# Kernel optimization log

Hardware: AMD Instinct MI355X
Metric: run time of the kernel (lower is better)

Reference implementation:

```python
import jax, jax.numpy as jnp
import numpy as np

N = 16000      # points
K = 16         # neighbors per query (fixed-degree CSR)
M = N * K      # attention pairs
C = 384        # embed_dim
H = 6          # num_heads
HD = C // H    # head_dim = 64
L = 25         # quant_grid_length = window/quant = 6.0/0.24
T2 = 2 * L - 1 # rel-pos table length = 49
WIN = 6.0
QUANT = 0.24
SCALE = HD ** -0.5


def setup_inputs() -> dict:
    key = jax.random.key(0)
    ks = jax.random.split(key, 12)
    feats = jax.random.normal(ks[0], (N, C), jnp.float32)
    xyz = jax.random.uniform(ks[1], (N, 3), jnp.float32) * 240.0
    index_0 = jnp.repeat(jnp.arange(N, dtype=jnp.int32), K)            # sorted query ids per pair
    index_0_offsets = jnp.arange(0, M + 1, K, dtype=jnp.int32)         # CSR offsets
    index_1 = jax.random.randint(ks[2], (M,), 0, N, jnp.int32)         # key ids per pair
    sort_idx = jax.random.permutation(ks[3], N).astype(jnp.int32)
    lin = lambda k: jax.random.normal(k, (C, C), jnp.float32) * 0.02
    tab = lambda k: jax.random.normal(k, (T2, 3, H, HD), jnp.float32) * 0.02
    return {
        'feats': feats, 'xyz': xyz,
        'index_0': index_0, 'index_0_offsets': index_0_offsets,
        'index_1': index_1, 'sort_idx': sort_idx,
        'Wq': lin(ks[4]), 'bq': jnp.zeros((C,), jnp.float32),
        'Wk': lin(ks[5]), 'bk': jnp.zeros((C,), jnp.float32),
        'Wv': lin(ks[6]), 'bv': jnp.zeros((C,), jnp.float32),
        'Wp': lin(ks[7]), 'bp': jnp.zeros((C,), jnp.float32),
        'Tq': tab(ks[8]), 'Tk': tab(ks[9]), 'Tv': tab(ks[10]),
    }


def reference(feats, xyz, index_0, index_0_offsets, index_1, sort_idx,
              Wq, bq, Wk, bk, Wv, bv, Wp, bp, Tq, Tk, Tv):
    n = feats.shape[0]
    # QKV projections (key/value default to query feats in the module)
    q = (feats @ Wq.T + bq).reshape(n, H, HD) * SCALE
    k = (feats @ Wk.T + bk).reshape(n, H, HD)
    v = (feats @ Wv.T + bv).reshape(n, H, HD)
    # sort into contiguous-window order
    qs, ks_, vs = q[sort_idx], k[sort_idx], v[sort_idx]
    xyz_s = xyz[sort_idx]
    # quantized in-window coords (shift_win=False -> shift 0)
    xq = jnp.floor(((xyz_s - xyz_s.min(0)) % WIN) / QUANT)             # [N,3], values in [0, L-1]
    i0, i1 = index_0, index_1
    rel_idx = (xq[i0] - xq[i1]).astype(jnp.int32) + (L - 1)            # [M,3] in [0, 2L-2]
    # attention logits: q.k plus contextual relative-position terms
    attn = jnp.einsum('mhd,mhd->mh', qs[i0], ks_[i1])                  # [M,H]
    for t in range(3):
        dq = jnp.einsum('nhd,lhd->nlh', qs, Tq[:, t])                  # [N,T2,H]
        dk = jnp.einsum('nhd,lhd->nlh', ks_, Tk[:, t])
        attn = attn + dq[i0, rel_idx[:, t]] + dk[i1, rel_idx[:, t]]
    # scatter softmax over CSR segments (segments given by index_0)
    amax = jax.ops.segment_max(attn, i0, num_segments=n)
    e = jnp.exp(attn - amax[i0])
    denom = jax.ops.segment_sum(e, i0, num_segments=n)
    a = e / denom[i0]                                                  # [M,H]
    # weighted value aggregation
    x = jax.ops.segment_sum(a[:, :, None] * vs[i1], i0, num_segments=n)  # [N,H,HD]
    # relative-position value contribution, factored through table bins
    for t in range(3):
        seg2 = i0 * T2 + rel_idx[:, t]
        w = jax.ops.segment_sum(a, seg2, num_segments=n * T2).reshape(n, T2, H)
        x = x + jnp.einsum('nlh,lhd->nhd', w, Tv[:, t])
    # unsort back to input order and project
    out = jnp.zeros_like(x).at[sort_idx].set(x).reshape(n, C)
    return out @ Wp.T + bp
```

## Files before the change

### kernel.cpp

```cpp
#include <hip/hip_runtime.h>
#include <hip/hip_bf16.h>
#include <cstdint>
#include <cstddef>

#define NPTS 16000
#define KNB  16
#define CDIM 384
#define NH   6
#define HDIM 64
#define T2C  49
#define NL3T 147
#define DQPAD 896
#define NXC  2944

static constexpr float WIN    = 6.0f;
static constexpr float QUANT  = 0.24f;
static constexpr float QSCALE = 0.125f;

typedef __attribute__((ext_vector_type(8))) short short8;
typedef __attribute__((ext_vector_type(4))) float floatx4;
typedef __attribute__((ext_vector_type(4))) unsigned short ushort4v;

__device__ inline unsigned short f2bf(float x) {
    unsigned int u = __float_as_uint(x);
    unsigned int r = (u + 0x7fffu + ((u >> 16) & 1u)) >> 16;
    return (unsigned short)r;
}
__device__ inline float bf2f(unsigned short b) {
    return __uint_as_float(((unsigned int)b) << 16);
}

__global__ void init_min_kernel(unsigned int* minbits) {
    if (threadIdx.x < 3) minbits[threadIdx.x] = 0x7f800000u;
}

__global__ void min_kernel(const float* __restrict__ xyz,
                           unsigned int* __restrict__ minbits) {
    float m0 = INFINITY, m1 = INFINITY, m2 = INFINITY;
    for (int i = blockIdx.x * blockDim.x + threadIdx.x; i < NPTS;
         i += gridDim.x * blockDim.x) {
        m0 = fminf(m0, xyz[i * 3 + 0]);
        m1 = fminf(m1, xyz[i * 3 + 1]);
        m2 = fminf(m2, xyz[i * 3 + 2]);
    }
#pragma unroll
    for (int off = 1; off < 64; off <<= 1) {
        m0 = fminf(m0, __shfl_xor(m0, off, 64));
        m1 = fminf(m1, __shfl_xor(m1, off, 64));
        m2 = fminf(m2, __shfl_xor(m2, off, 64));
    }
    if ((threadIdx.x & 63) == 0) {
        atomicMin(&minbits[0], __float_as_uint(m0));
        atomicMin(&minbits[1], __float_as_uint(m1));
        atomicMin(&minbits[2], __float_as_uint(m2));
    }
}

__global__ void xq_kernel(const float* __restrict__ xyz,
                          const int* __restrict__ sort_idx,
                          const unsigned int* __restrict__ minbits,
                          int* __restrict__ xq) {
    int n = blockIdx.x * blockDim.x + threadIdx.x;
    if (n >= NPTS) return;
    int orig = sort_idx[n];
#pragma unroll
    for (int t = 0; t < 3; ++t) {
        float mn = __uint_as_float(minbits[t]);
        float v  = xyz[orig * 3 + t] - mn;
        float md = fmodf(v, WIN);
        float q  = floorf(md / QUANT);
        xq[n * 3 + t] = (int)q;
    }
}

__global__ void relpack_kernel(const int* __restrict__ idx1,
                               const int* __restrict__ xq,
                               unsigned int* __restrict__ pairs) {
    int m = blockIdx.x * blockDim.x + threadIdx.x;
    if (m >= NPTS * KNB) return;
    int n = m >> 4;
    int key = idx1[m];
    int r0 = xq[n * 3 + 0] - xq[key * 3 + 0] + 24; r0 = min(max(r0, 0), T2C - 1);
    int r1 = xq[n * 3 + 1] - xq[key * 3 + 1] + 24; r1 = min(max(r1, 0), T2C - 1);
    int r2 = xq[n * 3 + 2] - xq[key * 3 + 2] + 24; r2 = min(max(r2, 0), T2C - 1);
    pairs[m] = (unsigned)key | ((unsigned)r0 << 14) | ((unsigned)r1 << 20) |
               ((unsigned)r2 << 26);
}

#define G0 (NPTS * CDIM / 4)
#define G1 (3 * CDIM * CDIM)
#define G2 (CDIM * CDIM)
#define G3 (NL3T * NH * HDIM)
#define G4 (3 * CDIM)
#define G5 (CDIM)
__global__ void prep_kernel(const float* __restrict__ feats,
                            const int* __restrict__ sortix,
                            const float* __restrict__ Wq,
                            const float* __restrict__ Wk,
                            const float* __restrict__ Wv,
                            const float* __restrict__ Wp,
                            const float* __restrict__ bq,
                            const float* __restrict__ bk,
                            const float* __restrict__ bv,
                            const float* __restrict__ bp,
                            const float* __restrict__ Tv,
                            unsigned short* __restrict__ featsbf,
                            unsigned short* __restrict__ Wall,
                            unsigned short* __restrict__ Wpbf,
                            unsigned short* __restrict__ Tvbf,
                            float* __restrict__ bfull,
                            float* __restrict__ bproj) {
    int i = blockIdx.x * blockDim.x + threadIdx.x;
    if (i < G0) {
        int n  = i / (CDIM / 4);
        int c4 = (i % (CDIM / 4)) * 4;
        const float4 v = *(const float4*)&feats[(size_t)sortix[n] * CDIM + c4];
        ushort4v o;
        o.x = f2bf(v.x); o.y = f2bf(v.y); o.z = f2bf(v.z); o.w = f2bf(v.w);
        *(ushort4v*)&featsbf[(size_t)n * CDIM + c4] = o;
        return;
    }
    i -= G0;
    if (i < G1) {
        int j = i / CDIM, k = i % CDIM;
        float v = (j < 384) ? Wq[j * CDIM + k]
                : (j < 768) ? Wk[(j - 384) * CDIM + k]
                            : Wv[(j - 768) * CDIM + k];
        Wall[i] = f2bf(v);
        return;
    }
    i -= G1;
    if (i < G2) { Wpbf[i] = f2bf(Wp[i]); return; }
    i -= G2;
    if (i < G3) { Tvbf[i] = f2bf(Tv[i]); return; }
    i -= G3;
    if (i < G4) {
        bfull[i] = (i < 384) ? bq[i] : (i < 768) ? bk[i - 384] : bv[i - 768];
        return;
    }
    i -= G4;
    if (i < G5) { bproj[i] = bp[i]; }
}

__global__ __launch_bounds__(384) void weff_kernel(
    const float* __restrict__ Wq, const float* __restrict__ Wk,
    const float* __restrict__ bq, const float* __restrict__ bk,
    const float* __restrict__ Tq, const float* __restrict__ Tk,
    unsigned short* __restrict__ Wall, float* __restrict__ bfull) {
    const int rr   = blockIdx.x;
    const bool isk = blockIdx.y != 0;
    const int base = isk ? 2048 : 1152;
    const float sc = isk ? 1.0f : QSCALE;
    const float* W = isk ? Wk : Wq;
    const float* bv = isk ? bk : bq;
    const float* T = isk ? Tk : Tq;
    const int c = threadIdx.x;

    if (rr >= NL3T * NH) {
        Wall[(size_t)(base + rr) * CDIM + c] = 0;
        if (c == 0) bfull[base + rr] = 0.0f;
        return;
    }
    const int h = rr % NH;

    __shared__ float Trow[HDIM];
    if (c < HDIM) Trow[c] = T[(size_t)rr * HDIM + c];
    __syncthreads();

    float acc = 0.0f;
#pragma unroll
    for (int d = 0; d < HDIM; ++d)
        acc += Trow[d] * W[(size_t)(h * HDIM + d) * CDIM + c];
    Wall[(size_t)(base + rr) * CDIM + c] = f2bf(acc * sc);

    if (c == 0) {
        float bacc = 0.0f;
#pragma unroll
        for (int d = 0; d < HDIM; ++d) bacc += Trow[d] * bv[h * HDIM + d];
        bfull[base + rr] = bacc * sc;
    }
}

__global__ __launch_bounds__(256) void gemm_big(
    const unsigned short* __restrict__ Abf,
    const unsigned short* __restrict__ Wmat,
    const float* __restrict__ bias,
    int mode, int nxout,
    unsigned short* __restrict__ QX, float* __restrict__ outf) {
    __shared__ unsigned short As[128 * 64];
    __shared__ unsigned short Bs[128 * 64];
    const int tid  = threadIdx.x;
    const int lane = tid & 63;
    const int w    = tid >> 6;
    const int wm   = w >> 1, wn = w & 1;
    const int jn0  = blockIdx.x * 128;
    const int m0   = blockIdx.y * 128;

    floatx4 acc[4][4];
#pragma unroll
    for (int i = 0; i < 4; ++i)
#pragma unroll
        for (int j = 0; j < 4; ++j) acc[i][j] = (floatx4)0.0f;

    for (int kt = 0; kt < 6; ++kt) {
        const int k0 = kt * 64;
#pragma unroll
        for (int q = 0; q < 4; ++q) {
            const int s    = w * 4 + q;
            const int row  = s * 8 + (lane >> 3);
            const int col  = (lane & 7) * 8;
            const unsigned short* ga = Abf  + (size_t)(m0  + row) * CDIM + k0 + col;
            const unsigned short* gb = Wmat + (size_t)(jn0 + row) * CDIM + k0 + col;
            __builtin_amdgcn_global_load_lds(
                (const __attribute__((address_space(1))) void*)ga,
                (__attribute__((address_space(3))) void*)&As[s * 512], 16, 0, 0);
            __builtin_amdgcn_global_load_lds(
                (const __attribute__((address_space(1))) void*)gb,
                (__attribute__((address_space(3))) void*)&Bs[s * 512], 16, 0, 0);
        }
        __syncthreads();
#pragma unroll
        for (int ks = 0; ks < 2; ++ks) {
            short8 a[4], b[4];
#pragma unroll
            for (int mi = 0; mi < 4; ++mi) {
                int row = wm * 64 + mi * 16 + (lane & 15);
                a[mi] = *(const short8*)&As[row * 64 + ks * 32 + (lane >> 4) * 8];
            }
#pragma unroll
            for (int ni = 0; ni < 4; ++ni) {
                int jr = wn * 64 + ni * 16 + (lane & 15);
                b[ni] = *(const short8*)&Bs[jr * 64 + ks * 32 + (lane >> 4) * 8];
            }
#pragma unroll
            for (int mi = 0; mi < 4; ++mi)
#pragma unroll
                for (int ni = 0; ni < 4; ++ni)
                    acc[mi][ni] = __builtin_amdgcn_mfma_f32_16x16x32_bf16(
                        b[ni], a[mi], acc[mi][ni], 0, 0, 0);
        }
        __syncthreads();
    }

#pragma unroll
    for (int mi = 0; mi < 4; ++mi) {
        const int n = m0 + wm * 64 + mi * 16 + (lane & 15);
#pragma unroll
        for (int ni = 0; ni < 4; ++ni) {
            const int jjb = jn0 + wn * 64 + ni * 16 + (lane >> 4) * 4;
            const float4 b4 = *(const float4*)&bias[jjb];
            if (mode == 0) {
                const float scl = (jjb < 384) ? QSCALE : 1.0f;
                ushort4v o;
                o.x = f2bf((acc[mi][ni][0] + b4.x) * scl);
                o.y = f2bf((acc[mi][ni][1] + b4.y) * scl);
                o.z = f2bf((acc[mi][ni][2] + b4.z) * scl);
                o.w = f2bf((acc[mi][ni][3] + b4.w) * scl);
                *(ushort4v*)&QX[(size_t)n * nxout + jjb] = o;
            } else {
                float4 o;
                o.x = acc[mi][ni][0] + b4.x;
                o.y = acc[mi][ni][1] + b4.y;
                o.z = acc[mi][ni][2] + b4.z;
                o.w = acc[mi][ni][3] + b4.w;
                *(float4*)&outf[(size_t)n * nxout + jjb] = o;
            }
        }
    }
}

__global__ __launch_bounds__(384) void attn_kernel(
    const unsigned short* __restrict__ QX,
    const unsigned int* __restrict__ pairs,
    const unsigned short* __restrict__ Tvbf,
    const int* __restrict__ sortix,
    unsigned short* __restrict__ xb) {
    const int n    = blockIdx.x;
    const int h    = threadIdx.x >> 6;
    const int lane = threadIdx.x & 63;
    const int pp   = lane >> 4, c = lane & 15;

    const unsigned short* qrow = QX + (size_t)n * NXC;
    const ushort4v q4 = *(const ushort4v*)&qrow[h * HDIM + c * 4];
    const float qx = bf2f(q4.x), qy = bf2f(q4.y), qz = bf2f(q4.z), qw = bf2f(q4.w);

    unsigned int pv[4];
#pragma unroll
    for (int g = 0; g < 4; ++g) pv[g] = pairs[n * KNB + g * 4 + pp];

    const unsigned short* krow[4];
    int j0g[4], j1g[4], j2g[4];
#pragma unroll
    for (int g = 0; g < 4; ++g) {
        krow[g] = QX + (size_t)(pv[g] & 0x3FFFu) * NXC;
        j0g[g]  = (int)((pv[g] >> 14) & 63u) * 18;
        j1g[g]  = (int)((pv[g] >> 20) & 63u) * 18 + 6;
        j2g[g]  = (int)(pv[g] >> 26) * 18 + 12;
    }

    float tab[4];
#pragma unroll
    for (int g = 0; g < 4; ++g) {
        tab[g] = bf2f(qrow[1152 + j0g[g] + h]) + bf2f(qrow[1152 + j1g[g] + h]) +
                 bf2f(qrow[1152 + j2g[g] + h]) +
                 bf2f(krow[g][2048 + j0g[g] + h]) + bf2f(krow[g][2048 + j1g[g] + h]) +
                 bf2f(krow[g][2048 + j2g[g] + h]);
    }

    float lg[4];
#pragma unroll
    for (int g = 0; g < 4; ++g) {
        const ushort4v k4 = *(const ushort4v*)&krow[g][384 + h * HDIM + c * 4];
        lg[g] = qx * bf2f(k4.x) + qy * bf2f(k4.y) + qz * bf2f(k4.z) + qw * bf2f(k4.w);
    }
#pragma unroll
    for (int m = 1; m <= 8; m <<= 1)
#pragma unroll
        for (int g = 0; g < 4; ++g) lg[g] += __shfl_xor(lg[g], m, 64);
#pragma unroll
    for (int g = 0; g < 4; ++g) lg[g] += tab[g];

    float mx = fmaxf(fmaxf(lg[0], lg[1]), fmaxf(lg[2], lg[3]));
    mx = fmaxf(mx, __shfl_xor(mx, 16, 64));
    mx = fmaxf(mx, __shfl_xor(mx, 32, 64));
    float e[4], s = 0.f;
#pragma unroll
    for (int g = 0; g < 4; ++g) { e[g] = expf(lg[g] - mx); s += e[g]; }
    s += __shfl_xor(s, 16, 64);
    s += __shfl_xor(s, 32, 64);
    const float inv = 1.f / s;

    float xa0 = 0.f, xa1 = 0.f, xa2 = 0.f, xa3 = 0.f;
#pragma unroll
    for (int g = 0; g < 4; ++g) {
        const float wgt = e[g] * inv;
        const ushort4v v4 = *(const ushort4v*)&krow[g][768 + h * HDIM + c * 4];
        const ushort4v t0 = *(const ushort4v*)&Tvbf[(size_t)(j0g[g] + h) * HDIM + c * 4];
        const ushort4v t1 = *(const ushort4v*)&Tvbf[(size_t)(j1g[g] + h) * HDIM + c * 4];
        const ushort4v t2 = *(const ushort4v*)&Tvbf[(size_t)(j2g[g] + h) * HDIM + c * 4];
        xa0 += wgt * (bf2f(v4.x) + bf2f(t0.x) + bf2f(t1.x) + bf2f(t2.x));
        xa1 += wgt * (bf2f(v4.y) + bf2f(t0.y) + bf2f(t1.y) + bf2f(t2.y));
        xa2 += wgt * (bf2f(v4.z) + bf2f(t0.z) + bf2f(t1.z) + bf2f(t2.z));
        xa3 += wgt * (bf2f(v4.w) + bf2f(t0.w) + bf2f(t1.w) + bf2f(t2.w));
    }
#pragma unroll
    for (int m = 16; m <= 32; m <<= 1) {
        xa0 += __shfl_xor(xa0, m, 64);
        xa1 += __shfl_xor(xa1, m, 64);
        xa2 += __shfl_xor(xa2, m, 64);
        xa3 += __shfl_xor(xa3, m, 64);
    }
    if (pp == 0) {
        const int dst = sortix[n];
        ushort4v o;
        o.x = f2bf(xa0); o.y = f2bf(xa1); o.z = f2bf(xa2); o.w = f2bf(xa3);
        *(ushort4v*)&xb[(size_t)dst * CDIM + h * HDIM + c * 4] = o;
    }
}

extern "C" void kernel_launch(void* const* d_in, const int* in_sizes, int n_in,
                              void* d_out, int out_size, void* d_ws,
                              size_t ws_size, hipStream_t stream) {
    const float* feats  = (const float*)d_in[0];
    const float* xyz    = (const float*)d_in[1];
    const int*   index1 = (const int*)d_in[4];
    const int*   sortix = (const int*)d_in[5];
    const float* Wq = (const float*)d_in[6];
    const float* bq = (const float*)d_in[7];
    const float* Wk = (const float*)d_in[8];
    const float* bk = (const float*)d_in[9];
    const float* Wv = (const float*)d_in[10];
    const float* bv = (const float*)d_in[11];
    const float* Wp = (const float*)d_in[12];
    const float* bp = (const float*)d_in[13];
    const float* Tq = (const float*)d_in[14];
    const float* Tk = (const float*)d_in[15];
    const float* Tv = (const float*)d_in[16];
    float* out = (float*)d_out;

    char* ws = (char*)d_ws;
    size_t off = 0;
    auto alloc = [&](size_t bytes) -> void* {
        void* p = ws + off;
        off = (off + bytes + 255) & ~(size_t)255;
        return p;
    };
    unsigned short* featsbf = (unsigned short*)alloc((size_t)NPTS * CDIM * 2);
    unsigned short* Wall    = (unsigned short*)alloc((size_t)NXC * CDIM * 2);
    unsigned short* Wpbf    = (unsigned short*)alloc((size_t)CDIM * CDIM * 2);
    unsigned short* Tvbf    = (unsigned short*)alloc((size_t)NL3T * NH * HDIM * 2);
    float*          bfull   = (float*)alloc((size_t)NXC * sizeof(float));
    float*          bproj   = (float*)alloc((size_t)CDIM * sizeof(float));
    unsigned short* QX      = (unsigned short*)alloc((size_t)NPTS * NXC * 2);
    unsigned int*   pairs   = (unsigned int*)alloc((size_t)NPTS * KNB * 4);
    int*            xq      = (int*)alloc((size_t)NPTS * 3 * sizeof(int));
    unsigned int*   minbits = (unsigned int*)alloc(16);
    unsigned short* xb      = featsbf;

    init_min_kernel<<<1, 64, 0, stream>>>(minbits);
    min_kernel<<<128, 256, 0, stream>>>(xyz, minbits);
    xq_kernel<<<(NPTS + 255) / 256, 256, 0, stream>>>(xyz, sortix, minbits, xq);
    relpack_kernel<<<(NPTS * KNB + 255) / 256, 256, 0, stream>>>(index1, xq, pairs);

    const int prep_total = G0 + G1 + G2 + G3 + G4 + G5;
    prep_kernel<<<(prep_total + 255) / 256, 256, 0, stream>>>(
        feats, sortix, Wq, Wk, Wv, Wp, bq, bk, bv, bp, Tv,
        featsbf, Wall, Wpbf, Tvbf, bfull, bproj);

    dim3 gw(DQPAD, 2);
    weff_kernel<<<gw, 384, 0, stream>>>(Wq, Wk, bq, bk, Tq, Tk, Wall, bfull);

    dim3 g0(NXC / 128, NPTS / 128);
    gemm_big<<<g0, 256, 0, stream>>>(featsbf, Wall, bfull, 0, NXC, QX,
                                     (float*)nullptr);

    attn_kernel<<<NPTS, 384, 0, stream>>>(QX, pairs, Tvbf, sortix, xb);

    dim3 g1(CDIM / 128, NPTS / 128);
    gemm_big<<<g1, 256, 0, stream>>>(xb, Wpbf, bproj, 1, CDIM,
                                     (unsigned short*)nullptr, out);
}
```

Measured before the change: 237.6 us.

## Store positional dot tables in fp8, enlarge GEMM tiles, remap workgroups across XCDs

The projected relative-position score columns (dq/dk tables) are now written as scaled fp8 in a 4096-byte padded row layout, while q/k/v stay bf16. This shrinks the largest intermediate and the gather traffic in the attention kernel. The GEMM moves to 256x128 tiles with 512 threads, pads M to 16128, and remaps workgroup ids so neighbouring tiles land on the same XCD. The fp8 storage adds quantization error to the attention logits, and the padded rows add extra work that is thrown away.

```diff
diff --git a/kernel.cpp b/kernel.cpp
--- a/kernel.cpp
+++ b/kernel.cpp
@@ -4,6 +4,7 @@
 #include <cstddef>
 
 #define NPTS 16000
+#define MPAD 16128
 #define KNB  16
 #define CDIM 384
 #define NH   6
@@ -12,10 +13,13 @@
 #define NL3T 147
 #define DQPAD 896
 #define NXC  2944
+#define ROWB 4096
 
 static constexpr float WIN    = 6.0f;
 static constexpr float QUANT  = 0.24f;
 static constexpr float QSCALE = 0.125f;
+static constexpr float DQS    = 8.0f;
+static constexpr float DQSINV = 0.125f;
 
 typedef __attribute__((ext_vector_type(8))) short short8;
 typedef __attribute__((ext_vector_type(4))) float floatx4;
@@ -28,6 +32,9 @@
 }
 __device__ inline float bf2f(unsigned short b) {
     return __uint_as_float(((unsigned int)b) << 16);
+}
+__device__ inline float f8tof(unsigned char b) {
+    return __builtin_amdgcn_cvt_f32_fp8((int)b, 0);
 }
 
 __global__ void init_min_kernel(unsigned int* minbits) {
@@ -150,7 +157,7 @@
     const int rr   = blockIdx.x;
     const bool isk = blockIdx.y != 0;
     const int base = isk ? 2048 : 1152;
-    const float sc = isk ? 1.0f : QSCALE;
+    const float sc = (isk ? 1.0f : QSCALE) * DQS;
     const float* W = isk ? Wk : Wq;
     const float* bv = isk ? bk : bq;
     const float* T = isk ? Tk : Tq;
@@ -181,20 +188,26 @@
     }
 }
 
-__global__ __launch_bounds__(256) void gemm_big(
+__global__ __launch_bounds__(512) void gemm_big(
     const unsigned short* __restrict__ Abf,
     const unsigned short* __restrict__ Wmat,
     const float* __restrict__ bias,
-    int mode, int nxout,
-    unsigned short* __restrict__ QX, float* __restrict__ outf) {
-    __shared__ unsigned short As[128 * 64];
+    int mode,
+    unsigned char* __restrict__ QXb, float* __restrict__ outf) {
+    __shared__ unsigned short As[256 * 64];
     __shared__ unsigned short Bs[128 * 64];
     const int tid  = threadIdx.x;
     const int lane = tid & 63;
     const int w    = tid >> 6;
     const int wm   = w >> 1, wn = w & 1;
-    const int jn0  = blockIdx.x * 128;
-    const int m0   = blockIdx.y * 128;
+
+    const int nwg  = gridDim.x * gridDim.y;
+    const int orig = blockIdx.y * gridDim.x + blockIdx.x;
+    const int qq   = nwg >> 3, rr = nwg & 7;
+    const int xcd  = orig & 7, idx = orig >> 3;
+    const int wg   = (xcd < rr ? xcd * (qq + 1) : rr * (qq + 1) + (xcd - rr) * qq) + idx;
+    const int jn0  = (wg % gridDim.x) * 128;
+    const int m0   = (wg / gridDim.x) * 256;
 
     floatx4 acc[4][4];
 #pragma unroll
@@ -204,16 +217,21 @@
 
     for (int kt = 0; kt < 6; ++kt) {
         const int k0 = kt * 64;
+        const int col = (lane & 7) * 8;
 #pragma unroll
         for (int q = 0; q < 4; ++q) {
-            const int s    = w * 4 + q;
-            const int row  = s * 8 + (lane >> 3);
-            const int col  = (lane & 7) * 8;
-            const unsigned short* ga = Abf  + (size_t)(m0  + row) * CDIM + k0 + col;
-            const unsigned short* gb = Wmat + (size_t)(jn0 + row) * CDIM + k0 + col;
+            const int s   = w * 4 + q;
+            const int row = s * 8 + (lane >> 3);
+            const unsigned short* ga = Abf + (size_t)(m0 + row) * CDIM + k0 + col;
             __builtin_amdgcn_global_load_lds(
                 (const __attribute__((address_space(1))) void*)ga,
                 (__attribute__((address_space(3))) void*)&As[s * 512], 16, 0, 0);
+        }
+#pragma unroll
+        for (int q = 0; q < 2; ++q) {
+            const int s   = w * 2 + q;
+            const int row = s * 8 + (lane >> 3);
+            const unsigned short* gb = Wmat + (size_t)(jn0 + row) * CDIM + k0 + col;
             __builtin_amdgcn_global_load_lds(
                 (const __attribute__((address_space(1))) void*)gb,
                 (__attribute__((address_space(3))) void*)&Bs[s * 512], 16, 0, 0);
@@ -249,28 +267,35 @@
         for (int ni = 0; ni < 4; ++ni) {
             const int jjb = jn0 + wn * 64 + ni * 16 + (lane >> 4) * 4;
             const float4 b4 = *(const float4*)&bias[jjb];
+            const float v0 = acc[mi][ni][0] + b4.x;
+            const float v1 = acc[mi][ni][1] + b4.y;
+            const float v2 = acc[mi][ni][2] + b4.z;
+            const float v3 = acc[mi][ni][3] + b4.w;
             if (mode == 0) {
-                const float scl = (jjb < 384) ? QSCALE : 1.0f;
-                ushort4v o;
-                o.x = f2bf((acc[mi][ni][0] + b4.x) * scl);
-                o.y = f2bf((acc[mi][ni][1] + b4.y) * scl);
-                o.z = f2bf((acc[mi][ni][2] + b4.z) * scl);
-                o.w = f2bf((acc[mi][ni][3] + b4.w) * scl);
-                *(ushort4v*)&QX[(size_t)n * nxout + jjb] = o;
+                unsigned char* rowb = QXb + (size_t)n * ROWB;
+                if (jjb < 1152) {
+                    const float scl = (jjb < 384) ? QSCALE : 1.0f;
+                    ushort4v o;
+                    o.x = f2bf(v0 * scl); o.y = f2bf(v1 * scl);
+                    o.z = f2bf(v2 * scl); o.w = f2bf(v3 * scl);
+                    *(ushort4v*)(rowb + jjb * 2) = o;
+                } else {
+                    int u = __builtin_amdgcn_cvt_pk_fp8_f32(v0, v1, 0, false);
+                    u = __builtin_amdgcn_cvt_pk_fp8_f32(v2, v3, u, true);
+                    *(unsigned int*)(rowb + jjb + 1152) = (unsigned int)u;
+                }
             } else {
-                float4 o;
-                o.x = acc[mi][ni][0] + b4.x;
-                o.y = acc[mi][ni][1] + b4.y;
-                o.z = acc[mi][ni][2] + b4.z;
-                o.w = acc[mi][ni][3] + b4.w;
-                *(float4*)&outf[(size_t)n * nxout + jjb] = o;
+                if (n < NPTS) {
+                    float4 o; o.x = v0; o.y = v1; o.z = v2; o.w = v3;
+                    *(float4*)&outf[(size_t)n * CDIM + jjb] = o;
+                }
             }
         }
     }
 }
 
 __global__ __launch_bounds__(384) void attn_kernel(
-    const unsigned short* __restrict__ QX,
+    const unsigned char* __restrict__ QXb,
     const unsigned int* __restrict__ pairs,
     const unsigned short* __restrict__ Tvbf,
     const int* __restrict__ sortix,
@@ -280,19 +305,19 @@
     const int lane = threadIdx.x & 63;
     const int pp   = lane >> 4, c = lane & 15;
 
-    const unsigned short* qrow = QX + (size_t)n * NXC;
-    const ushort4v q4 = *(const ushort4v*)&qrow[h * HDIM + c * 4];
+    const unsigned char* qrow = QXb + (size_t)n * ROWB;
+    const ushort4v q4 = *(const ushort4v*)(qrow + h * 128 + c * 8);
     const float qx = bf2f(q4.x), qy = bf2f(q4.y), qz = bf2f(q4.z), qw = bf2f(q4.w);
 
     unsigned int pv[4];
 #pragma unroll
     for (int g = 0; g < 4; ++g) pv[g] = pairs[n * KNB + g * 4 + pp];
 
-    const unsigned short* krow[4];
+    const unsigned char* krow[4];
     int j0g[4], j1g[4], j2g[4];
 #pragma unroll
     for (int g = 0; g < 4; ++g) {
-        krow[g] = QX + (size_t)(pv[g] & 0x3FFFu) * NXC;
+        krow[g] = QXb + (size_t)(pv[g] & 0x3FFFu) * ROWB;
         j0g[g]  = (int)((pv[g] >> 14) & 63u) * 18;
         j1g[g]  = (int)((pv[g] >> 20) & 63u) * 18 + 6;
         j2g[g]  = (int)(pv[g] >> 26) * 18 + 12;
@@ -301,16 +326,17 @@
     float tab[4];
 #pragma unroll
     for (int g = 0; g < 4; ++g) {
-        tab[g] = bf2f(qrow[1152 + j0g[g] + h]) + bf2f(qrow[1152 + j1g[g] + h]) +
-                 bf2f(qrow[1152 + j2g[g] + h]) +
-                 bf2f(krow[g][2048 + j0g[g] + h]) + bf2f(krow[g][2048 + j1g[g] + h]) +
-                 bf2f(krow[g][2048 + j2g[g] + h]);
+        tab[g] = DQSINV *
+            (f8tof(qrow[2304 + j0g[g] + h]) + f8tof(qrow[2304 + j1g[g] + h]) +
+             f8tof(qrow[2304 + j2g[g] + h]) +
+             f8tof(krow[g][3200 + j0g[g] + h]) + f8tof(krow[g][3200 + j1g[g] + h]) +
+             f8tof(krow[g][3200 + j2g[g] + h]));
     }
 
     float lg[4];
 #pragma unroll
     for (int g = 0; g < 4; ++g) {
-        const ushort4v k4 = *(const ushort4v*)&krow[g][384 + h * HDIM + c * 4];
+        const ushort4v k4 = *(const ushort4v*)(krow[g] + 768 + h * 128 + c * 8);
         lg[g] = qx * bf2f(k4.x) + qy * bf2f(k4.y) + qz * bf2f(k4.z) + qw * bf2f(k4.w);
     }
 #pragma unroll
@@ -334,7 +360,7 @@
 #pragma unroll
     for (int g = 0; g < 4; ++g) {
         const float wgt = e[g] * inv;
-        const ushort4v v4 = *(const ushort4v*)&krow[g][768 + h * HDIM + c * 4];
+        const ushort4v v4 = *(const ushort4v*)(krow[g] + 1536 + h * 128 + c * 8);
         const ushort4v t0 = *(const ushort4v*)&Tvbf[(size_t)(j0g[g] + h) * HDIM + c * 4];
         const ushort4v t1 = *(const ushort4v*)&Tvbf[(size_t)(j1g[g] + h) * HDIM + c * 4];
         const ushort4v t2 = *(const ushort4v*)&Tvbf[(size_t)(j2g[g] + h) * HDIM + c * 4];
@@ -385,13 +411,13 @@
         off = (off + bytes + 255) & ~(size_t)255;
         return p;
     };
-    unsigned short* featsbf = (unsigned short*)alloc((size_t)NPTS * CDIM * 2);
+    unsigned short* featsbf = (unsigned short*)alloc((size_t)MPAD * CDIM * 2);
     unsigned short* Wall    = (unsigned short*)alloc((size_t)NXC * CDIM * 2);
     unsigned short* Wpbf    = (unsigned short*)alloc((size_t)CDIM * CDIM * 2);
     unsigned short* Tvbf    = (unsigned short*)alloc((size_t)NL3T * NH * HDIM * 2);
     float*          bfull   = (float*)alloc((size_t)NXC * sizeof(float));
     float*          bproj   = (float*)alloc((size_t)CDIM * sizeof(float));
-    unsigned short* QX      = (unsigned short*)alloc((size_t)NPTS * NXC * 2);
+    unsigned char*  QXb     = (unsigned char*)alloc((size_t)MPAD * ROWB);
     unsigned int*   pairs   = (unsigned int*)alloc((size_t)NPTS * KNB * 4);
     int*            xq      = (int*)alloc((size_t)NPTS * 3 * sizeof(int));
     unsigned int*   minbits = (unsigned int*)alloc(16);
@@ -410,13 +436,13 @@
     dim3 gw(DQPAD, 2);
     weff_kernel<<<gw, 384, 0, stream>>>(Wq, Wk, bq, bk, Tq, Tk, Wall, bfull);
 
-    dim3 g0(NXC / 128, NPTS / 128);
-    gemm_big<<<g0, 256, 0, stream>>>(featsbf, Wall, bfull, 0, NXC, QX,
+    dim3 g0(NXC / 128, MPAD / 256);
+    gemm_big<<<g0, 512, 0, stream>>>(featsbf, Wall, bfull, 0, QXb,
                                      (float*)nullptr);
 
-    attn_kernel<<<NPTS, 384, 0, stream>>>(QX, pairs, Tvbf, sortix, xb);
-
-    dim3 g1(CDIM / 128, NPTS / 128);
-    gemm_big<<<g1, 256, 0, stream>>>(xb, Wpbf, bproj, 1, CDIM,
-                                     (unsigned short*)nullptr, out);
-}
+    attn_kernel<<<NPTS, 384, 0, stream>>>(QXb, pairs, Tvbf, sortix, xb);
+
+    dim3 g1(CDIM / 128, MPAD / 256);
+    gemm_big<<<g1, 512, 0, stream>>>(xb, Wpbf, bproj, 1, (unsigned char*)nullptr,
+                                     out);
+}
```

Result: slower. 253.8 us (+6.8%).
